# Kernel tuning notes

Measured on AMD Instinct MI355X. Metric: run time of the kernel, lower is better.

The kernel has to match this reference:

```python
import jax, jax.numpy as jnp
import numpy as np
from jax import lax

IN_PLANES = 512
GROWTH = 32
PLANES = 4 * GROWTH  # 128
EPS = 1e-5


def setup_inputs() -> dict:
    key = jax.random.key(0)
    ks = jax.random.split(key, 10)
    x = jax.random.normal(ks[0], (128, IN_PLANES, 32, 32), dtype=jnp.float32)
    # bn1 affine params (batch-stat BN, track_running_stats=False)
    gamma1 = jax.random.normal(ks[1], (IN_PLANES,), dtype=jnp.float32) * 0.1 + 1.0
    beta1 = jax.random.normal(ks[2], (IN_PLANES,), dtype=jnp.float32) * 0.1
    # convbn1: 1x1 conv weight + folded BN (running stats)
    w1 = jax.random.normal(ks[3], (PLANES, IN_PLANES, 1, 1), dtype=jnp.float32) * (1.0 / np.sqrt(IN_PLANES))
    gamma2 = jax.random.normal(ks[4], (PLANES,), dtype=jnp.float32) * 0.1 + 1.0
    beta2 = jax.random.normal(ks[5], (PLANES,), dtype=jnp.float32) * 0.1
    mean2 = jax.random.normal(ks[6], (PLANES,), dtype=jnp.float32) * 0.1
    var2 = jax.random.uniform(ks[7], (PLANES,), dtype=jnp.float32, minval=0.5, maxval=1.5)
    # conv2: 3x3 conv, padding 1, no bias
    w2 = jax.random.normal(ks[8], (GROWTH, PLANES, 3, 3), dtype=jnp.float32) * (1.0 / np.sqrt(9 * PLANES))
    return {"x": x, "gamma1": gamma1, "beta1": beta1, "w1": w1,
            "gamma2": gamma2, "beta2": beta2, "mean2": mean2, "var2": var2,
            "w2": w2}


def _bn(h, mean, var, gamma, beta):
    # channel-wise affine normalization, NCHW
    inv = lax.rsqrt(var + EPS)
    scale = (gamma * inv)[None, :, None, None]
    shift = (beta - mean * gamma * inv)[None, :, None, None]
    return h * scale + shift


def reference(x, gamma1, beta1, w1, gamma2, beta2, mean2, var2, w2):
    # bn1: batch statistics (track_running_stats=False)
    mu = jnp.mean(x, axis=(0, 2, 3))
    var = jnp.var(x, axis=(0, 2, 3))  # biased, as torch BN normalization
    h = _bn(x, mu, var, gamma1, beta1)
    h = jax.nn.relu(h)
    # convbn1: 1x1 conv then folded BN (running stats)
    h = lax.conv_general_dilated(h, w1, (1, 1), 'VALID',
                                 dimension_numbers=('NCHW', 'OIHW', 'NCHW'))
    h = _bn(h, mean2, var2, gamma2, beta2)
    h = jax.nn.relu(h)
    # conv2: 3x3, stride 1, pad 1, no bias
    out = lax.conv_general_dilated(h, w2, (1, 1), ((1, 1), (1, 1)),
                                   dimension_numbers=('NCHW', 'OIHW', 'NCHW'))
    # dense concat along channels
    return jnp.concatenate([x, out], axis=1)
```

## Files before the change

kernel.cpp:

```cpp
#include <hip/hip_runtime.h>

#define EPS 1e-5f

typedef __bf16 bf16x8 __attribute__((ext_vector_type(8)));
typedef unsigned short ushort8 __attribute__((ext_vector_type(8)));
typedef float f32x4 __attribute__((ext_vector_type(4)));

static __device__ __forceinline__ unsigned short f2bf(float f) {
  unsigned int u = __float_as_uint(f);
  u += 0x7fffu + ((u >> 16) & 1u);
  return (unsigned short)(u >> 16);
}


__global__ void prep_kernel(const float* __restrict__ w1,
                            const float* __restrict__ gamma2,
                            const float* __restrict__ beta2,
                            const float* __restrict__ mean2,
                            const float* __restrict__ var2,
                            const float* __restrict__ w2,
                            unsigned short* __restrict__ w1b,
                            unsigned short* __restrict__ w2b,
                            float* __restrict__ bias2) {
  int idx = blockIdx.x * 256 + threadIdx.x;
  if (idx < 128 * 512) {
    int oc = idx >> 9;
    float s2 = gamma2[oc] * rsqrtf(var2[oc] + EPS);
    w1b[idx] = f2bf(w1[idx] * s2);
  } else if (idx < 128 * 512 + 32 * 1152) {
    int i2 = idx - 128 * 512;
    int oc = i2 / 1152;
    int rem = i2 - oc * 1152;
    int tap = rem >> 7;
    int c = rem & 127;
    w2b[i2] = f2bf(w2[(oc * 128 + c) * 9 + tap]);
  } else if (idx < 128 * 512 + 32 * 1152 + 128) {
    int oc = idx - (128 * 512 + 32 * 1152);
    float s2 = gamma2[oc] * rsqrtf(var2[oc] + EPS);
    bias2[oc] = beta2[oc] - mean2[oc] * s2;
  }
}

__global__ void __launch_bounds__(256) stats_copy_kernel(
    const float* __restrict__ x, const float* __restrict__ g1,
    const float* __restrict__ be1, float* __restrict__ out,
    float* __restrict__ s1, float* __restrict__ b1) {
  const int c = blockIdx.x;
  const int t = threadIdx.x;
  float sum = 0.f, sq = 0.f;
  const float4* __restrict__ x4 = (const float4*)x;
  float4* out4 = (float4*)out;
  for (int n = 0; n < 128; ++n) {
    float4 v = x4[(((size_t)n * 512 + c) << 8) + t];
    out4[(((size_t)n * 544 + c) << 8) + t] = v;
    sum += v.x + v.y + v.z + v.w;
    sq += v.x * v.x + v.y * v.y + v.z * v.z + v.w * v.w;
  }
  __shared__ float ls[2][4];
  for (int off = 32; off > 0; off >>= 1) {
    sum += __shfl_down(sum, off);
    sq += __shfl_down(sq, off);
  }
  int w = t >> 6;
  if ((t & 63) == 0) { ls[0][w] = sum; ls[1][w] = sq; }
  __syncthreads();
  if (t == 0) {
    float S = ls[0][0] + ls[0][1] + ls[0][2] + ls[0][3];
    float Q = ls[1][0] + ls[1][1] + ls[1][2] + ls[1][3];
    float mean = S * (1.0f / 131072.0f);
    float var = Q * (1.0f / 131072.0f) - mean * mean;
    float s = g1[c] * rsqrtf(var + EPS);
    s1[c] = s;
    b1[c] = be1[c] - mean * s;
  }
}

__global__ void __launch_bounds__(256, 2) conv1_kernel(
    const float* __restrict__ x, const unsigned short* __restrict__ w1b,
    const float* __restrict__ s1, const float* __restrict__ b1,
    const float* __restrict__ bias2, unsigned short* __restrict__ h2) {
  const int t = threadIdx.x;
  const int lane = t & 63;
  const int wv = t >> 6;
  const int n = blockIdx.x >> 2;
  const int p0w = (blockIdx.x & 3) * 256 + wv * 64;
  const int l15 = lane & 15;
  const int kb = lane >> 4;

  f32x4 acc[8][4];
#pragma unroll
  for (int m = 0; m < 8; ++m)
#pragma unroll
    for (int g = 0; g < 4; ++g) acc[m][g] = (f32x4){0.f, 0.f, 0.f, 0.f};

  const float* __restrict__ xn = x + (size_t)n * 512 * 1024;

  for (int c0 = 0; c0 < 512; c0 += 32) {
    const int cbase = c0 + kb * 8;
    float s1v[8], b1v[8];
#pragma unroll
    for (int j = 0; j < 8; ++j) {
      s1v[j] = s1[cbase + j];
      b1v[j] = b1[cbase + j];
    }
    bf16x8 bf[4];
#pragma unroll
    for (int g = 0; g < 4; ++g) {
      const int p = p0w + g * 16 + l15;
      ushort8 tmp;
#pragma unroll
      for (int j = 0; j < 8; ++j) {
        float xv = xn[(size_t)(cbase + j) * 1024 + p];
        float a = fmaxf(fmaf(xv, s1v[j], b1v[j]), 0.f);
        tmp[j] = f2bf(a);
      }
      bf[g] = __builtin_bit_cast(bf16x8, tmp);
    }
#pragma unroll
    for (int m = 0; m < 8; ++m) {
      bf16x8 af = *(const bf16x8*)(w1b + (size_t)(m * 16 + l15) * 512 + cbase);
#pragma unroll
      for (int g = 0; g < 4; ++g)
        acc[m][g] = __builtin_amdgcn_mfma_f32_16x16x32_bf16(af, bf[g], acc[m][g], 0, 0, 0);
    }
  }

#pragma unroll
  for (int m = 0; m < 8; ++m) {
    const int ocb = m * 16 + kb * 4;
    float bz0 = bias2[ocb + 0], bz1 = bias2[ocb + 1];
    float bz2 = bias2[ocb + 2], bz3 = bias2[ocb + 3];
#pragma unroll
    for (int g = 0; g < 4; ++g) {
      const int p = p0w + g * 16 + l15;
      ushort4 hv;
      hv.x = f2bf(fmaxf(acc[m][g][0] + bz0, 0.f));
      hv.y = f2bf(fmaxf(acc[m][g][1] + bz1, 0.f));
      hv.z = f2bf(fmaxf(acc[m][g][2] + bz2, 0.f));
      hv.w = f2bf(fmaxf(acc[m][g][3] + bz3, 0.f));
      *(ushort4*)(h2 + ((size_t)n * 1024 + p) * 128 + ocb) = hv;
    }
  }
}

__global__ void __launch_bounds__(256) conv2_kernel(
    const unsigned short* __restrict__ h2, const unsigned short* __restrict__ w2b,
    float* __restrict__ out) {
  const int t = threadIdx.x;
  const int lane = t & 63;
  const int wv = t >> 6;
  const int n = blockIdx.x >> 2;
  const int pbase = (blockIdx.x & 3) * 256 + wv * 64;
  const int l15 = lane & 15;
  const int kb = lane >> 4;

  f32x4 acc[2][4];
#pragma unroll
  for (int m = 0; m < 2; ++m)
#pragma unroll
    for (int g = 0; g < 4; ++g) acc[m][g] = (f32x4){0.f, 0.f, 0.f, 0.f};

  const unsigned short* __restrict__ h2n = h2 + (size_t)n * 1024 * 128;

#pragma unroll
  for (int tap = 0; tap < 9; ++tap) {
    const int dy = tap / 3 - 1;
    const int dx = tap % 3 - 1;
#pragma unroll
    for (int c0 = 0; c0 < 128; c0 += 32) {
      const int cb = c0 + kb * 8;
      bf16x8 af[2];
#pragma unroll
      for (int m = 0; m < 2; ++m)
        af[m] = *(const bf16x8*)(w2b + (size_t)(m * 16 + l15) * 1152 + tap * 128 + cb);
#pragma unroll
      for (int g = 0; g < 4; ++g) {
        const int p = pbase + g * 16 + l15;
        const int y = (p >> 5) & 31;
        const int xx = p & 31;
        const int y2 = y + dy;
        const int x2 = xx + dx;
        bf16x8 bv = __builtin_bit_cast(bf16x8, (ushort8){0, 0, 0, 0, 0, 0, 0, 0});
        if (y2 >= 0 && y2 < 32 && x2 >= 0 && x2 < 32)
          bv = *(const bf16x8*)(h2n + ((size_t)(y2 * 32 + x2)) * 128 + cb);
#pragma unroll
        for (int m = 0; m < 2; ++m)
          acc[m][g] = __builtin_amdgcn_mfma_f32_16x16x32_bf16(af[m], bv, acc[m][g], 0, 0, 0);
      }
    }
  }

#pragma unroll
  for (int m = 0; m < 2; ++m) {
    const int oc = m * 16 + kb * 4;
#pragma unroll
    for (int g = 0; g < 4; ++g) {
      const int p = pbase + g * 16 + l15;
#pragma unroll
      for (int r = 0; r < 4; ++r)
        out[((size_t)n * 544 + 512 + oc + r) * 1024 + p] = acc[m][g][r];
    }
  }
}

extern "C" void kernel_launch(void* const* d_in, const int* in_sizes, int n_in,
                              void* d_out, int out_size, void* d_ws, size_t ws_size,
                              hipStream_t stream) {
  const float* x = (const float*)d_in[0];
  const float* gamma1 = (const float*)d_in[1];
  const float* beta1 = (const float*)d_in[2];
  const float* w1 = (const float*)d_in[3];
  const float* gamma2 = (const float*)d_in[4];
  const float* beta2 = (const float*)d_in[5];
  const float* mean2 = (const float*)d_in[6];
  const float* var2 = (const float*)d_in[7];
  const float* w2 = (const float*)d_in[8];
  float* out = (float*)d_out;

  char* ws = (char*)d_ws;
  unsigned short* h2 = (unsigned short*)ws;
  unsigned short* w1b = (unsigned short*)(ws + 33554432);
  unsigned short* w2b = (unsigned short*)(ws + 33685504);
  float* s1 = (float*)(ws + 33759232);
  float* b1 = (float*)(ws + 33761280);
  float* bias2 = (float*)(ws + 33763328);

  prep_kernel<<<401, 256, 0, stream>>>(w1, gamma2, beta2, mean2, var2, w2, w1b, w2b, bias2);
  stats_copy_kernel<<<512, 256, 0, stream>>>(x, gamma1, beta1, out, s1, b1);
  conv1_kernel<<<512, 256, 0, stream>>>(x, w1b, s1, b1, bias2, h2);
  conv2_kernel<<<512, 256, 0, stream>>>(h2, w2b, out);
}
```

Before: 223.0 us.

## Split BN stats over batch chunks, add nontemporal stores, reverse conv1 batch order

The stats/copy kernel now runs 4096 blocks, each covering 16 images of one channel, writing partial sums that a small new reduce kernel combines into the BN scale and shift. This replaces 512 long serial blocks with many short ones to use more CUs. Output stores in the copy and in conv2 become nontemporal to avoid polluting cache. conv1 walks the batch in reverse so the most recently copied images are more likely still cached, and the bf16 conversion switches to native casts. Risks are one extra launch and a slightly different summation order.

```diff
diff --git a/kernel.cpp b/kernel.cpp
--- a/kernel.cpp
+++ b/kernel.cpp
@@ -3,6 +3,7 @@
 #define EPS 1e-5f
 
 typedef __bf16 bf16x8 __attribute__((ext_vector_type(8)));
+typedef __bf16 bf16x4 __attribute__((ext_vector_type(4)));
 typedef unsigned short ushort8 __attribute__((ext_vector_type(8)));
 typedef float f32x4 __attribute__((ext_vector_type(4)));
 
@@ -42,31 +43,46 @@
 }
 
 __global__ void __launch_bounds__(256) stats_copy_kernel(
-    const float* __restrict__ x, const float* __restrict__ g1,
-    const float* __restrict__ be1, float* __restrict__ out,
-    float* __restrict__ s1, float* __restrict__ b1) {
-  const int c = blockIdx.x;
+    const float* __restrict__ x, float* __restrict__ out,
+    float* __restrict__ psum, float* __restrict__ psq) {
+  const int c = blockIdx.x & 511;
+  const int nq = blockIdx.x >> 9;
   const int t = threadIdx.x;
   float sum = 0.f, sq = 0.f;
-  const float4* __restrict__ x4 = (const float4*)x;
-  float4* out4 = (float4*)out;
-  for (int n = 0; n < 128; ++n) {
-    float4 v = x4[(((size_t)n * 512 + c) << 8) + t];
-    out4[(((size_t)n * 544 + c) << 8) + t] = v;
-    sum += v.x + v.y + v.z + v.w;
-    sq += v.x * v.x + v.y * v.y + v.z * v.z + v.w * v.w;
+  const f32x4* __restrict__ x4 = (const f32x4*)x;
+  f32x4* out4 = (f32x4*)out;
+#pragma unroll 4
+  for (int i = 0; i < 16; ++i) {
+    const int n = nq * 16 + i;
+    f32x4 v = x4[(((size_t)n * 512 + c) << 8) + t];
+    __builtin_nontemporal_store(v, &out4[(((size_t)n * 544 + c) << 8) + t]);
+    sum += v[0] + v[1] + v[2] + v[3];
+    sq += v[0] * v[0] + v[1] * v[1] + v[2] * v[2] + v[3] * v[3];
   }
   __shared__ float ls[2][4];
   for (int off = 32; off > 0; off >>= 1) {
     sum += __shfl_down(sum, off);
     sq += __shfl_down(sq, off);
   }
-  int w = t >> 6;
+  const int w = t >> 6;
   if ((t & 63) == 0) { ls[0][w] = sum; ls[1][w] = sq; }
   __syncthreads();
   if (t == 0) {
-    float S = ls[0][0] + ls[0][1] + ls[0][2] + ls[0][3];
-    float Q = ls[1][0] + ls[1][1] + ls[1][2] + ls[1][3];
+    psum[c * 8 + nq] = ls[0][0] + ls[0][1] + ls[0][2] + ls[0][3];
+    psq[c * 8 + nq] = ls[1][0] + ls[1][1] + ls[1][2] + ls[1][3];
+  }
+}
+
+__global__ void reduce_kernel(const float* __restrict__ psum,
+                              const float* __restrict__ psq,
+                              const float* __restrict__ g1,
+                              const float* __restrict__ be1,
+                              float* __restrict__ s1, float* __restrict__ b1) {
+  int c = blockIdx.x * 256 + threadIdx.x;
+  if (c < 512) {
+    float S = 0.f, Q = 0.f;
+#pragma unroll
+    for (int q = 0; q < 8; ++q) { S += psum[c * 8 + q]; Q += psq[c * 8 + q]; }
     float mean = S * (1.0f / 131072.0f);
     float var = Q * (1.0f / 131072.0f) - mean * mean;
     float s = g1[c] * rsqrtf(var + EPS);
@@ -82,7 +98,7 @@
   const int t = threadIdx.x;
   const int lane = t & 63;
   const int wv = t >> 6;
-  const int n = blockIdx.x >> 2;
+  const int n = 127 - (blockIdx.x >> 2);
   const int p0w = (blockIdx.x & 3) * 256 + wv * 64;
   const int l15 = lane & 15;
   const int kb = lane >> 4;
@@ -107,14 +123,14 @@
 #pragma unroll
     for (int g = 0; g < 4; ++g) {
       const int p = p0w + g * 16 + l15;
-      ushort8 tmp;
+      bf16x8 tmp;
 #pragma unroll
       for (int j = 0; j < 8; ++j) {
         float xv = xn[(size_t)(cbase + j) * 1024 + p];
         float a = fmaxf(fmaf(xv, s1v[j], b1v[j]), 0.f);
-        tmp[j] = f2bf(a);
+        tmp[j] = (__bf16)a;
       }
-      bf[g] = __builtin_bit_cast(bf16x8, tmp);
+      bf[g] = tmp;
     }
 #pragma unroll
     for (int m = 0; m < 8; ++m) {
@@ -133,12 +149,12 @@
 #pragma unroll
     for (int g = 0; g < 4; ++g) {
       const int p = p0w + g * 16 + l15;
-      ushort4 hv;
-      hv.x = f2bf(fmaxf(acc[m][g][0] + bz0, 0.f));
-      hv.y = f2bf(fmaxf(acc[m][g][1] + bz1, 0.f));
-      hv.z = f2bf(fmaxf(acc[m][g][2] + bz2, 0.f));
-      hv.w = f2bf(fmaxf(acc[m][g][3] + bz3, 0.f));
-      *(ushort4*)(h2 + ((size_t)n * 1024 + p) * 128 + ocb) = hv;
+      bf16x4 hv;
+      hv[0] = (__bf16)fmaxf(acc[m][g][0] + bz0, 0.f);
+      hv[1] = (__bf16)fmaxf(acc[m][g][1] + bz1, 0.f);
+      hv[2] = (__bf16)fmaxf(acc[m][g][2] + bz2, 0.f);
+      hv[3] = (__bf16)fmaxf(acc[m][g][3] + bz3, 0.f);
+      *(bf16x4*)(h2 + ((size_t)n * 1024 + p) * 128 + ocb) = hv;
     }
   }
 }
@@ -198,7 +214,8 @@
       const int p = pbase + g * 16 + l15;
 #pragma unroll
       for (int r = 0; r < 4; ++r)
-        out[((size_t)n * 544 + 512 + oc + r) * 1024 + p] = acc[m][g][r];
+        __builtin_nontemporal_store(
+            acc[m][g][r], &out[((size_t)n * 544 + 512 + oc + r) * 1024 + p]);
     }
   }
 }
@@ -224,9 +241,12 @@
   float* s1 = (float*)(ws + 33759232);
   float* b1 = (float*)(ws + 33761280);
   float* bias2 = (float*)(ws + 33763328);
+  float* psum = (float*)(ws + 33763840);
+  float* psq = (float*)(ws + 33780224);
 
   prep_kernel<<<401, 256, 0, stream>>>(w1, gamma2, beta2, mean2, var2, w2, w1b, w2b, bias2);
-  stats_copy_kernel<<<512, 256, 0, stream>>>(x, gamma1, beta1, out, s1, b1);
+  stats_copy_kernel<<<4096, 256, 0, stream>>>(x, out, psum, psq);
+  reduce_kernel<<<2, 256, 0, stream>>>(psum, psq, gamma1, beta1, s1, b1);
   conv1_kernel<<<512, 256, 0, stream>>>(x, w1b, s1, b1, bias2, h2);
   conv2_kernel<<<512, 256, 0, stream>>>(h2, w2b, out);
 }
```

After: 207.2 us. -7.1%, faster.
